# Kernel tuning notes

Measured on AMD Instinct MI355X. Metric: run time of the kernel, lower is better.

## Reference

```python
import jax, jax.numpy as jnp
import numpy as np

B, V, H, R, RULE_DIM, DK, GMLP_H, OUT = 4096, 8, 512, 16, 64, 32, 16, 512
TEMP = float(np.sqrt(DK))  # SelectAttention temperature = sqrt(d_k)
EPS = 1e-10


def gumbel_hard(logits, u, tau=1.0):
    # straight-through hard gumbel-softmax over last axis (F.gumbel_softmax hard=True)
    g = -jnp.log(-jnp.log(u + EPS) + EPS)
    y = jax.nn.softmax((logits + g) / tau, axis=-1)
    hard = jax.nn.one_hot(jnp.argmax(y, axis=-1), y.shape[-1], dtype=y.dtype)
    return hard + y - jax.lax.stop_gradient(y)


def setup_inputs() -> dict:
    key = jax.random.key(0)
    ks = jax.random.split(key, 16)
    s = lambda d: 1.0 / np.sqrt(d)
    return {
        "hidden": jax.random.normal(ks[0], (B, V, H), jnp.float32),
        "u_var": jax.random.uniform(ks[1], (B, V * V), jnp.float32),
        "u_rule": jax.random.uniform(ks[2], (B, R), jnp.float32),
        # variable_rule_select: shared query/key Linear(H, 32)
        "Wq": jax.random.normal(ks[3], (H, DK), jnp.float32) * s(H),
        "bq": jnp.zeros((DK,), jnp.float32),
        "Wk": jax.random.normal(ks[4], (H, DK), jnp.float32) * s(H),
        "bk": jnp.zeros((DK,), jnp.float32),
        # rule embeddings [R, rule_dim]
        "rule_emb": jax.random.normal(ks[5], (R, RULE_DIM), jnp.float32),
        # rule_select_: shared Linear(3H, 32) query, Linear(rule_dim, 32) key
        "Wq2": jax.random.normal(ks[6], (3 * H, DK), jnp.float32) * s(3 * H),
        "bq2": jnp.zeros((DK,), jnp.float32),
        "Wk2": jax.random.normal(ks[7], (RULE_DIM, DK), jnp.float32) * s(RULE_DIM),
        "bk2": jnp.zeros((DK,), jnp.float32),
        # rule_mlp = GroupMLP(2H -> 16 -> input_dim, num=R), GroupLinearLayer has no bias
        "W1": jax.random.normal(ks[8], (R, 2 * H, GMLP_H), jnp.float32) * s(2 * H),
        "W2": jax.random.normal(ks[9], (R, GMLP_H, OUT), jnp.float32) * s(GMLP_H),
    }


def reference(hidden, u_var, u_rule, Wq, bq, Wk, bk, rule_emb, Wq2, bq2, Wk2, bk2, W1, W2):
    b, v, h = hidden.shape
    # variable_rule_select(hidden, hidden): shared Linear projections, bmm scores
    q = hidden @ Wq + bq                                  # [B,V,dk]
    k = hidden @ Wk + bk                                  # [B,V,dk]
    scores = jnp.einsum('bid,bjd->bij', q, k) / TEMP      # [B,V,V]
    # hard gumbel-softmax over flattened V*V pair grid
    mask = gumbel_hard(scores.reshape(b, -1), u_var).reshape(b, v, v)
    mask = mask.transpose(0, 2, 1)                        # mask.permute(0,2,1)
    primary = mask.sum(axis=2)                            # [B,V] one-hot primary variable
    context = mask.sum(axis=1)                            # [B,V] one-hot context variable
    h_p = jnp.einsum('bv,bvh->bh', primary, hidden)       # gather primary slot
    h_c = jnp.einsum('bv,bvh->bh', context, hidden)       # gather context slot
    h_mean = hidden.mean(axis=1)
    # rule_select_: query from concat(primary, context, pooled state) [B,3H]
    q2 = jnp.concatenate([h_p, h_c, h_mean], axis=-1) @ Wq2 + bq2   # [B,dk]
    k2 = rule_emb @ Wk2 + bk2                                        # [R,dk]
    rscores = (q2 @ k2.T) / TEMP                                     # [B,R]
    rmask = gumbel_hard(rscores, u_rule)                             # [B,R] one-hot rule
    # rule_mlp: GroupMLP(2H->16->input_dim) over all rules, then hard dispatch
    comb = jnp.concatenate([h_p, h_c], axis=-1)                      # [B,2H]
    h1 = jax.nn.relu(jnp.einsum('bd,rde->bre', comb, W1))            # [B,R,16]
    rout = jnp.einsum('bre,reo->bro', h1, W2)                        # [B,R,out]
    rule_out = jnp.einsum('br,bro->bo', rmask, rout)                 # [B,out]
    # scatter result back to the selected primary variable slot
    out = primary[:, :, None] * rule_out[:, None, :]                 # [B,V,out]
    return out
```

## Files before the change

kernel.cpp:

```cpp
#include <hip/hip_runtime.h>

#define TEMP 5.656854249492380195f
#define EPSG 1e-10f

#define XSTR 68
#define WSTR 64

__launch_bounds__(256, 2)
__global__ void k1_kernel(const float* __restrict__ hidden,
                          const float* __restrict__ u_var,
                          const float* __restrict__ u_rule,
                          const float* __restrict__ Wq,
                          const float* __restrict__ bq,
                          const float* __restrict__ Wk,
                          const float* __restrict__ bk,
                          const float* __restrict__ rule_emb,
                          const float* __restrict__ Wk2,
                          const float* __restrict__ bk2,
                          const float* __restrict__ Wq2,
                          const float* __restrict__ bq2,
                          int* __restrict__ selbuf,
                          int* __restrict__ rselbuf) {
    const int tid = threadIdx.x;
    const int b0  = blockIdx.x * 8;

    __shared__ float4 smem4[(64 * XSTR + 64 * WSTR) / 4];
    float* smem = reinterpret_cast<float*>(smem4);
    float* xt = smem;
    float* wt = smem + 64 * XSTR;
    __shared__ float  hm[8 * 512];
    __shared__ float  sk2[512];
    __shared__ float4 part4[4][8][8];
    __shared__ float  s_q2[8][32];
    __shared__ int    ssel[8];

    for (int t = tid; t < 512; t += 256) {
        int r = t >> 5, d = t & 31;
        float acc = bk2[d];
        for (int h = 0; h < 64; ++h)
            acc += rule_emb[r * 64 + h] * Wk2[h * 32 + d];
        sk2[t] = acc;
    }

    const int tn = tid & 15;
    const int tm = tid >> 4;

    float4 acc0 = make_float4(0.f, 0.f, 0.f, 0.f);
    float4 acc1 = make_float4(0.f, 0.f, 0.f, 0.f);
    float4 acc2 = make_float4(0.f, 0.f, 0.f, 0.f);
    float4 acc3 = make_float4(0.f, 0.f, 0.f, 0.f);

    for (int c = 0; c < 8; ++c) {
        #pragma unroll
        for (int p = 0; p < 4; ++p) {
            int f   = p * 256 + tid;
            int row = f >> 4;
            int c4  = f & 15;
            int bb  = row >> 3, v = row & 7;
            float4 val = *reinterpret_cast<const float4*>(
                hidden + (size_t)(b0 + bb) * 4096 + v * 512 + c * 64 + c4 * 4);
            *reinterpret_cast<float4*>(&xt[row * XSTR + c4 * 4]) = val;
        }
        #pragma unroll
        for (int p = 0; p < 4; ++p) {
            int f  = p * 256 + tid;
            int k  = f >> 4;
            int n4 = f & 15;
            int h  = c * 64 + k;
            const float* src = (n4 < 8) ? (Wq + h * 32 + n4 * 4)
                                        : (Wk + h * 32 + (n4 - 8) * 4);
            *reinterpret_cast<float4*>(&wt[k * WSTR + n4 * 4]) =
                *reinterpret_cast<const float4*>(src);
        }
        __syncthreads();

        #pragma unroll 4
        for (int k4 = 0; k4 < 16; ++k4) {
            float4 x0 = *reinterpret_cast<const float4*>(&xt[(tm * 4 + 0) * XSTR + k4 * 4]);
            float4 x1 = *reinterpret_cast<const float4*>(&xt[(tm * 4 + 1) * XSTR + k4 * 4]);
            float4 x2 = *reinterpret_cast<const float4*>(&xt[(tm * 4 + 2) * XSTR + k4 * 4]);
            float4 x3 = *reinterpret_cast<const float4*>(&xt[(tm * 4 + 3) * XSTR + k4 * 4]);
            float4 w0 = *reinterpret_cast<const float4*>(&wt[(k4 * 4 + 0) * WSTR + tn * 4]);
            float4 w1 = *reinterpret_cast<const float4*>(&wt[(k4 * 4 + 1) * WSTR + tn * 4]);
            float4 w2 = *reinterpret_cast<const float4*>(&wt[(k4 * 4 + 2) * WSTR + tn * 4]);
            float4 w3 = *reinterpret_cast<const float4*>(&wt[(k4 * 4 + 3) * WSTR + tn * 4]);
            acc0.x += x0.x * w0.x + x0.y * w1.x + x0.z * w2.x + x0.w * w3.x;
            acc0.y += x0.x * w0.y + x0.y * w1.y + x0.z * w2.y + x0.w * w3.y;
            acc0.z += x0.x * w0.z + x0.y * w1.z + x0.z * w2.z + x0.w * w3.z;
            acc0.w += x0.x * w0.w + x0.y * w1.w + x0.z * w2.w + x0.w * w3.w;
            acc1.x += x1.x * w0.x + x1.y * w1.x + x1.z * w2.x + x1.w * w3.x;
            acc1.y += x1.x * w0.y + x1.y * w1.y + x1.z * w2.y + x1.w * w3.y;
            acc1.z += x1.x * w0.z + x1.y * w1.z + x1.z * w2.z + x1.w * w3.z;
            acc1.w += x1.x * w0.w + x1.y * w1.w + x1.z * w2.w + x1.w * w3.w;
            acc2.x += x2.x * w0.x + x2.y * w1.x + x2.z * w2.x + x2.w * w3.x;
            acc2.y += x2.x * w0.y + x2.y * w1.y + x2.z * w2.y + x2.w * w3.y;
            acc2.z += x2.x * w0.z + x2.y * w1.z + x2.z * w2.z + x2.w * w3.z;
            acc2.w += x2.x * w0.w + x2.y * w1.w + x2.z * w2.w + x2.w * w3.w;
            acc3.x += x3.x * w0.x + x3.y * w1.x + x3.z * w2.x + x3.w * w3.x;
            acc3.y += x3.x * w0.y + x3.y * w1.y + x3.z * w2.y + x3.w * w3.y;
            acc3.z += x3.x * w0.z + x3.y * w1.z + x3.z * w2.z + x3.w * w3.z;
            acc3.w += x3.x * w0.w + x3.y * w1.w + x3.z * w2.w + x3.w * w3.w;
        }

        {
            int bb = tid >> 5, hg = tid & 31;
            float m0 = 0.f, m1 = 0.f;
            #pragma unroll
            for (int v = 0; v < 8; ++v) {
                float2 x2 = *reinterpret_cast<const float2*>(&xt[(bb * 8 + v) * XSTR + hg * 2]);
                m0 += x2.x; m1 += x2.y;
            }
            hm[bb * 512 + c * 64 + hg * 2]     = m0 * 0.125f;
            hm[bb * 512 + c * 64 + hg * 2 + 1] = m1 * 0.125f;
        }
        __syncthreads();
    }

    {
        const float* bsrc = (tn < 8) ? (bq + tn * 4) : (bk + (tn - 8) * 4);
        float4 bias4 = *reinterpret_cast<const float4*>(bsrc);
        float4 r0, r1, r2, r3;
        r0.x = acc0.x + bias4.x; r0.y = acc0.y + bias4.y; r0.z = acc0.z + bias4.z; r0.w = acc0.w + bias4.w;
        r1.x = acc1.x + bias4.x; r1.y = acc1.y + bias4.y; r1.z = acc1.z + bias4.z; r1.w = acc1.w + bias4.w;
        r2.x = acc2.x + bias4.x; r2.y = acc2.y + bias4.y; r2.z = acc2.z + bias4.z; r2.w = acc2.w + bias4.w;
        r3.x = acc3.x + bias4.x; r3.y = acc3.y + bias4.y; r3.z = acc3.z + bias4.z; r3.w = acc3.w + bias4.w;
        float* sq = smem;
        *reinterpret_cast<float4*>(&sq[(tm * 4 + 0) * XSTR + tn * 4]) = r0;
        *reinterpret_cast<float4*>(&sq[(tm * 4 + 1) * XSTR + tn * 4]) = r1;
        *reinterpret_cast<float4*>(&sq[(tm * 4 + 2) * XSTR + tn * 4]) = r2;
        *reinterpret_cast<float4*>(&sq[(tm * 4 + 3) * XSTR + tn * 4]) = r3;
    }
    __syncthreads();

    {
        const float* sq = smem;
        const int w    = tid >> 6;
        const int lane = tid & 63;
        #pragma unroll
        for (int half = 0; half < 2; ++half) {
            const int bb = w + half * 4;
            const int b  = b0 + bb;
            const int i = lane >> 3, j = lane & 7;
            float s = 0.f;
            #pragma unroll
            for (int d4 = 0; d4 < 8; ++d4) {
                float4 qv = *reinterpret_cast<const float4*>(&sq[(bb * 8 + i) * XSTR + d4 * 4]);
                float4 kv = *reinterpret_cast<const float4*>(&sq[(bb * 8 + j) * XSTR + 32 + d4 * 4]);
                s += qv.x * kv.x + qv.y * kv.y + qv.z * kv.z + qv.w * kv.w;
            }
            s /= TEMP;
            float u = u_var[(size_t)b * 64 + lane];
            float g = -logf(-logf(u + EPSG) + EPSG);
            float pm = s + g;
            int idx = lane;
            #pragma unroll
            for (int off = 32; off >= 1; off >>= 1) {
                float pv = __shfl_xor(pm, off);
                int   pi = __shfl_xor(idx, off);
                if (pv > pm || (pv == pm && pi < idx)) { pm = pv; idx = pi; }
            }
            if (lane == 0) { selbuf[b] = idx; ssel[bb] = idx; }
        }
    }
    __syncthreads();

    {
        float* comb = smem;
        const float4* h4 = reinterpret_cast<const float4*>(hidden);
        #pragma unroll
        for (int p = 0; p < 8; ++p) {
            int f    = p * 256 + tid;
            int bb   = f >> 8, idx = f & 255;
            int half = idx >> 7, cc = idx & 127;
            int sv   = ssel[bb];
            int row  = half ? (sv >> 3) : (sv & 7);
            reinterpret_cast<float4*>(comb)[bb * 256 + idx] =
                h4[((size_t)(b0 + bb) * 8 + row) * 128 + cc];
        }
    }
    __syncthreads();

    {
        const float* comb = smem;
        const int d4 = tid & 7, s = tid >> 3;
        float4 acc[8];
        #pragma unroll
        for (int bb = 0; bb < 8; ++bb) acc[bb] = make_float4(0.f, 0.f, 0.f, 0.f);

        for (int kt = 0; kt < 6; ++kt) {
            float4 w[8];
            #pragma unroll
            for (int j = 0; j < 8; ++j)
                w[j] = *reinterpret_cast<const float4*>(
                    Wq2 + (size_t)(kt * 256 + s * 8 + j) * 32 + d4 * 4);
            #pragma unroll
            for (int bb = 0; bb < 8; ++bb) {
                const float* xsrc = (kt < 4) ? &comb[bb * 1024 + kt * 256]
                                             : &hm[bb * 512 + (kt - 4) * 256];
                #pragma unroll
                for (int j = 0; j < 8; ++j) {
                    float x = xsrc[s * 8 + j];
                    acc[bb].x += x * w[j].x;
                    acc[bb].y += x * w[j].y;
                    acc[bb].z += x * w[j].z;
                    acc[bb].w += x * w[j].w;
                }
            }
        }
        #pragma unroll
        for (int off = 8; off < 64; off <<= 1) {
            #pragma unroll
            for (int bb = 0; bb < 8; ++bb) {
                acc[bb].x += __shfl_xor(acc[bb].x, off);
                acc[bb].y += __shfl_xor(acc[bb].y, off);
                acc[bb].z += __shfl_xor(acc[bb].z, off);
                acc[bb].w += __shfl_xor(acc[bb].w, off);
            }
        }
        if ((s & 7) == 0) {
            #pragma unroll
            for (int bb = 0; bb < 8; ++bb) part4[tid >> 6][bb][d4] = acc[bb];
        }
    }
    __syncthreads();
    {
        const int bb = tid >> 5, col = tid & 31;
        float q2 = bq2[col];
        #pragma unroll
        for (int wv = 0; wv < 4; ++wv) {
            const float* pf = reinterpret_cast<const float*>(&part4[wv][bb][col >> 2]);
            q2 += pf[col & 3];
        }
        s_q2[bb][col] = q2;
    }
    __syncthreads();
    if (tid < 128) {
        const int bb = tid >> 4, r = tid & 15;
        const int b = b0 + bb;
        float sc = 0.f;
        #pragma unroll
        for (int d = 0; d < 32; ++d) sc += s_q2[bb][d] * sk2[r * 32 + d];
        sc /= TEMP;
        float u = u_rule[(size_t)b * 16 + r];
        float g = -logf(-logf(u + EPSG) + EPSG);
        float pm = sc + g;
        int idx = r;
        #pragma unroll
        for (int off = 8; off >= 1; off >>= 1) {
            float pv = __shfl_xor(pm, off, 16);
            int   pi = __shfl_xor(idx, off, 16);
            if (pv > pm || (pv == pm && pi < idx)) { pm = pv; idx = pi; }
        }
        if (r == 0) rselbuf[b] = idx;
    }
}

__launch_bounds__(256, 4)
__global__ void k3_kernel(const float* __restrict__ hidden,
                          const float* __restrict__ W1,
                          const float* __restrict__ W2,
                          const int* __restrict__ selbuf,
                          const int* __restrict__ rselbuf,
                          float* __restrict__ outbuf) {
    const int tid = threadIdx.x;
    const int b   = blockIdx.x;

    __shared__ float comb[1024];
    __shared__ float part[4][16];
    __shared__ float s_h1[16];
    __shared__ float s_rout[512];

    const int sv = selbuf[b];
    const int r  = rselbuf[b];
    const int js = sv & 7, cs = sv >> 3;

    {
        const float4* h4 = reinterpret_cast<const float4*>(hidden);
        float4 v;
        if (tid < 128) v = h4[((size_t)b * 8 + js) * 128 + tid];
        else           v = h4[((size_t)b * 8 + cs) * 128 + (tid - 128)];
        *reinterpret_cast<float4*>(&comb[tid * 4]) = v;
    }
    __syncthreads();

    {
        const int e  = tid & 15;
        const int sl = tid >> 4;
        const float* w1p = W1 + (size_t)r * 16384;
        float a = 0.f;
        for (int i = 0; i < 64; ++i) {
            int rr = i * 16 + sl;
            a += comb[rr] * w1p[rr * 16 + e];
        }
        a += __shfl_xor(a, 16);
        a += __shfl_xor(a, 32);
        if ((sl & 3) == 0) part[sl >> 2][e] = a;
    }
    __syncthreads();
    if (tid < 16)
        s_h1[tid] = fmaxf(part[0][tid] + part[1][tid] + part[2][tid] + part[3][tid], 0.f);
    __syncthreads();

    {
        const float* w2 = W2 + (size_t)r * 8192;
        int o0 = tid * 2;
        float a0 = 0.f, a1 = 0.f;
        #pragma unroll
        for (int ee = 0; ee < 16; ++ee) {
            float h1e = s_h1[ee];
            float2 ww = *reinterpret_cast<const float2*>(w2 + ee * 512 + o0);
            a0 += h1e * ww.x;
            a1 += h1e * ww.y;
        }
        s_rout[o0]     = a0;
        s_rout[o0 + 1] = a1;
    }
    __syncthreads();

    {
        const int v    = tid >> 5;
        const int col0 = (tid & 31) * 16;
        float4 z = make_float4(0.f, 0.f, 0.f, 0.f);
        float4 r0 = z, r1 = z, r2 = z, r3 = z;
        if (v == js) {
            r0 = *reinterpret_cast<const float4*>(&s_rout[col0]);
            r1 = *reinterpret_cast<const float4*>(&s_rout[col0 + 4]);
            r2 = *reinterpret_cast<const float4*>(&s_rout[col0 + 8]);
            r3 = *reinterpret_cast<const float4*>(&s_rout[col0 + 12]);
        }
        float* ob = outbuf + (size_t)b * 4096 + v * 512 + col0;
        *reinterpret_cast<float4*>(ob)      = r0;
        *reinterpret_cast<float4*>(ob + 4)  = r1;
        *reinterpret_cast<float4*>(ob + 8)  = r2;
        *reinterpret_cast<float4*>(ob + 12) = r3;
    }
}

extern "C" void kernel_launch(void* const* d_in, const int* in_sizes, int n_in,
                              void* d_out, int out_size, void* d_ws, size_t ws_size,
                              hipStream_t stream) {
    const float* hidden   = (const float*)d_in[0];
    const float* u_var    = (const float*)d_in[1];
    const float* u_rule   = (const float*)d_in[2];
    const float* Wq       = (const float*)d_in[3];
    const float* bq       = (const float*)d_in[4];
    const float* Wk       = (const float*)d_in[5];
    const float* bk       = (const float*)d_in[6];
    const float* rule_emb = (const float*)d_in[7];
    const float* Wq2      = (const float*)d_in[8];
    const float* bq2      = (const float*)d_in[9];
    const float* Wk2      = (const float*)d_in[10];
    const float* bk2      = (const float*)d_in[11];
    const float* W1       = (const float*)d_in[12];
    const float* W2       = (const float*)d_in[13];

    char* ws = (char*)d_ws;
    int*   sel  = (int*)(ws + 4096);
    int*   rsel = (int*)(ws + 20480);
    float* outf = (float*)d_out;

    hipLaunchKernelGGL(k1_kernel, dim3(512), dim3(256), 0, stream,
                       hidden, u_var, u_rule, Wq, bq, Wk, bk,
                       rule_emb, Wk2, bk2, Wq2, bq2, sel, rsel);
    hipLaunchKernelGGL(k3_kernel, dim3(4096), dim3(256), 0, stream,
                       hidden, W1, W2, sel, rsel, outf);
}
```

Before: 90.39 us.

## Double-buffer QK projection staging with direct global-to-LDS loads

Restructures the Q/K projection loop into 16 smaller 32-wide K chunks with two LDS buffers, issuing the next chunk's hidden and weight loads before computing on the current one. Where available it uses the global_load_lds builtin to write directly into shared memory without passing through registers. This aims to hide global-load latency behind the FMA loop, but it drops the padded row strides, which may bring back LDS bank conflicts, and the loop now runs twice as many iterations, each ending in a barrier.

```diff
diff --git a/kernel.cpp b/kernel.cpp
--- a/kernel.cpp
+++ b/kernel.cpp
@@ -3,8 +3,26 @@
 #define TEMP 5.656854249492380195f
 #define EPSG 1e-10f
 
-#define XSTR 68
-#define WSTR 64
+#define KCH 32
+
+#if defined(__has_builtin)
+#if __has_builtin(__builtin_amdgcn_global_load_lds)
+#define HAVE_GLL 1
+#endif
+#endif
+
+__device__ __forceinline__ void stage_f4(const float* gp, float* lp_base, int lane) {
+#ifdef HAVE_GLL
+    (void)lane;
+    __builtin_amdgcn_global_load_lds(
+        (const __attribute__((address_space(1))) unsigned int*)(gp),
+        (__attribute__((address_space(3))) unsigned int*)(lp_base),
+        16, 0, 0);
+#else
+    float4 v = *reinterpret_cast<const float4*>(gp);
+    *reinterpret_cast<float4*>(lp_base + lane * 4) = v;
+#endif
+}
 
 __launch_bounds__(256, 2)
 __global__ void k1_kernel(const float* __restrict__ hidden,
@@ -24,11 +42,8 @@
     const int tid = threadIdx.x;
     const int b0  = blockIdx.x * 8;
 
-    __shared__ float4 smem4[(64 * XSTR + 64 * WSTR) / 4];
-    float* smem = reinterpret_cast<float*>(smem4);
-    float* xt = smem;
-    float* wt = smem + 64 * XSTR;
-    __shared__ float  hm[8 * 512];
+    __shared__ float  smem[8192];
+    __shared__ float  hm[4096];
     __shared__ float  sk2[512];
     __shared__ float4 part4[4][8][8];
     __shared__ float  s_q2[8][32];
@@ -42,48 +57,59 @@
         sk2[t] = acc;
     }
 
-    const int tn = tid & 15;
-    const int tm = tid >> 4;
+    const int w    = tid >> 6;
+    const int lane = tid & 63;
+    const int tn   = tid & 15;
+    const int tm   = tid >> 4;
 
     float4 acc0 = make_float4(0.f, 0.f, 0.f, 0.f);
     float4 acc1 = make_float4(0.f, 0.f, 0.f, 0.f);
     float4 acc2 = make_float4(0.f, 0.f, 0.f, 0.f);
     float4 acc3 = make_float4(0.f, 0.f, 0.f, 0.f);
 
-    for (int c = 0; c < 8; ++c) {
-        #pragma unroll
-        for (int p = 0; p < 4; ++p) {
-            int f   = p * 256 + tid;
-            int row = f >> 4;
-            int c4  = f & 15;
-            int bb  = row >> 3, v = row & 7;
-            float4 val = *reinterpret_cast<const float4*>(
-                hidden + (size_t)(b0 + bb) * 4096 + v * 512 + c * 64 + c4 * 4);
-            *reinterpret_cast<float4*>(&xt[row * XSTR + c4 * 4]) = val;
-        }
-        #pragma unroll
-        for (int p = 0; p < 4; ++p) {
-            int f  = p * 256 + tid;
-            int k  = f >> 4;
-            int n4 = f & 15;
-            int h  = c * 64 + k;
-            const float* src = (n4 < 8) ? (Wq + h * 32 + n4 * 4)
-                                        : (Wk + h * 32 + (n4 - 8) * 4);
-            *reinterpret_cast<float4*>(&wt[k * WSTR + n4 * 4]) =
-                *reinterpret_cast<const float4*>(src);
-        }
-        __syncthreads();
+    #define STAGE_CHUNK(c_, p_)                                               \
+    do {                                                                      \
+        _Pragma("unroll")                                                     \
+        for (int i = 0; i < 2; ++i) {                                         \
+            int f   = w * 128 + i * 64 + lane;            \
+            int row = f >> 3, c4 = f & 7;                                     \
+            const float* gp = hidden + (size_t)(b0 + (row >> 3)) * 4096       \
+                              + (row & 7) * 512 + (c_) * KCH + c4 * 4;        \
+            stage_f4(gp, &smem[(p_) * 4096 + (w * 128 + i * 64) * 4], lane);  \
+        }                                                                     \
+        _Pragma("unroll")                                                     \
+        for (int i = 0; i < 2; ++i) {                                         \
+            int f  = w * 128 + i * 64 + lane;             \
+            int k  = f >> 4, n4 = f & 15;                                     \
+            const float* gp = (n4 < 8)                                        \
+                ? (Wq + (size_t)((c_) * KCH + k) * 32 + n4 * 4)               \
+                : (Wk + (size_t)((c_) * KCH + k) * 32 + (n4 - 8) * 4);        \
+            stage_f4(gp, &smem[(p_) * 4096 + 2048 + (w * 128 + i * 64) * 4],  \
+                     lane);                                                   \
+        }                                                                     \
+    } while (0)
+
+    STAGE_CHUNK(0, 0);
+    __syncthreads();
+
+    for (int c = 0; c < 16; ++c) {
+        const int p = c & 1;
+
+        if (c < 15) STAGE_CHUNK(c + 1, p ^ 1);
+
+        const float* xt = &smem[p * 4096];
+        const float* wt = &smem[p * 4096 + 2048];
 
         #pragma unroll 4
-        for (int k4 = 0; k4 < 16; ++k4) {
-            float4 x0 = *reinterpret_cast<const float4*>(&xt[(tm * 4 + 0) * XSTR + k4 * 4]);
-            float4 x1 = *reinterpret_cast<const float4*>(&xt[(tm * 4 + 1) * XSTR + k4 * 4]);
-            float4 x2 = *reinterpret_cast<const float4*>(&xt[(tm * 4 + 2) * XSTR + k4 * 4]);
-            float4 x3 = *reinterpret_cast<const float4*>(&xt[(tm * 4 + 3) * XSTR + k4 * 4]);
-            float4 w0 = *reinterpret_cast<const float4*>(&wt[(k4 * 4 + 0) * WSTR + tn * 4]);
-            float4 w1 = *reinterpret_cast<const float4*>(&wt[(k4 * 4 + 1) * WSTR + tn * 4]);
-            float4 w2 = *reinterpret_cast<const float4*>(&wt[(k4 * 4 + 2) * WSTR + tn * 4]);
-            float4 w3 = *reinterpret_cast<const float4*>(&wt[(k4 * 4 + 3) * WSTR + tn * 4]);
+        for (int k4 = 0; k4 < 8; ++k4) {
+            float4 x0 = *reinterpret_cast<const float4*>(&xt[(tm * 4 + 0) * 32 + k4 * 4]);
+            float4 x1 = *reinterpret_cast<const float4*>(&xt[(tm * 4 + 1) * 32 + k4 * 4]);
+            float4 x2 = *reinterpret_cast<const float4*>(&xt[(tm * 4 + 2) * 32 + k4 * 4]);
+            float4 x3 = *reinterpret_cast<const float4*>(&xt[(tm * 4 + 3) * 32 + k4 * 4]);
+            float4 w0 = *reinterpret_cast<const float4*>(&wt[(k4 * 4 + 0) * 64 + tn * 4]);
+            float4 w1 = *reinterpret_cast<const float4*>(&wt[(k4 * 4 + 1) * 64 + tn * 4]);
+            float4 w2 = *reinterpret_cast<const float4*>(&wt[(k4 * 4 + 2) * 64 + tn * 4]);
+            float4 w3 = *reinterpret_cast<const float4*>(&wt[(k4 * 4 + 3) * 64 + tn * 4]);
             acc0.x += x0.x * w0.x + x0.y * w1.x + x0.z * w2.x + x0.w * w3.x;
             acc0.y += x0.x * w0.y + x0.y * w1.y + x0.z * w2.y + x0.w * w3.y;
             acc0.z += x0.x * w0.z + x0.y * w1.z + x0.z * w2.z + x0.w * w3.z;
@@ -104,14 +130,10 @@
 
         {
             int bb = tid >> 5, hg = tid & 31;
-            float m0 = 0.f, m1 = 0.f;
-            #pragma unroll
-            for (int v = 0; v < 8; ++v) {
-                float2 x2 = *reinterpret_cast<const float2*>(&xt[(bb * 8 + v) * XSTR + hg * 2]);
-                m0 += x2.x; m1 += x2.y;
-            }
-            hm[bb * 512 + c * 64 + hg * 2]     = m0 * 0.125f;
-            hm[bb * 512 + c * 64 + hg * 2 + 1] = m1 * 0.125f;
+            float m = 0.f;
+            #pragma unroll
+            for (int v = 0; v < 8; ++v) m += xt[(bb * 8 + v) * 32 + hg];
+            hm[bb * 512 + c * KCH + hg] = m * 0.125f;
         }
         __syncthreads();
     }
@@ -125,17 +147,15 @@
         r2.x = acc2.x + bias4.x; r2.y = acc2.y + bias4.y; r2.z = acc2.z + bias4.z; r2.w = acc2.w + bias4.w;
         r3.x = acc3.x + bias4.x; r3.y = acc3.y + bias4.y; r3.z = acc3.z + bias4.z; r3.w = acc3.w + bias4.w;
         float* sq = smem;
-        *reinterpret_cast<float4*>(&sq[(tm * 4 + 0) * XSTR + tn * 4]) = r0;
-        *reinterpret_cast<float4*>(&sq[(tm * 4 + 1) * XSTR + tn * 4]) = r1;
-        *reinterpret_cast<float4*>(&sq[(tm * 4 + 2) * XSTR + tn * 4]) = r2;
-        *reinterpret_cast<float4*>(&sq[(tm * 4 + 3) * XSTR + tn * 4]) = r3;
+        *reinterpret_cast<float4*>(&sq[(tm * 4 + 0) * 64 + tn * 4]) = r0;
+        *reinterpret_cast<float4*>(&sq[(tm * 4 + 1) * 64 + tn * 4]) = r1;
+        *reinterpret_cast<float4*>(&sq[(tm * 4 + 2) * 64 + tn * 4]) = r2;
+        *reinterpret_cast<float4*>(&sq[(tm * 4 + 3) * 64 + tn * 4]) = r3;
     }
     __syncthreads();
 
     {
         const float* sq = smem;
-        const int w    = tid >> 6;
-        const int lane = tid & 63;
         #pragma unroll
         for (int half = 0; half < 2; ++half) {
             const int bb = w + half * 4;
@@ -144,8 +164,8 @@
             float s = 0.f;
             #pragma unroll
             for (int d4 = 0; d4 < 8; ++d4) {
-                float4 qv = *reinterpret_cast<const float4*>(&sq[(bb * 8 + i) * XSTR + d4 * 4]);
-                float4 kv = *reinterpret_cast<const float4*>(&sq[(bb * 8 + j) * XSTR + 32 + d4 * 4]);
+                float4 qv = *reinterpret_cast<const float4*>(&sq[(bb * 8 + i) * 64 + d4 * 4]);
+                float4 kv = *reinterpret_cast<const float4*>(&sq[(bb * 8 + j) * 64 + 32 + d4 * 4]);
                 s += qv.x * kv.x + qv.y * kv.y + qv.z * kv.z + qv.w * kv.w;
             }
             s /= TEMP;
@@ -188,10 +208,10 @@
         for (int bb = 0; bb < 8; ++bb) acc[bb] = make_float4(0.f, 0.f, 0.f, 0.f);
 
         for (int kt = 0; kt < 6; ++kt) {
-            float4 w[8];
+            float4 wv[8];
             #pragma unroll
             for (int j = 0; j < 8; ++j)
-                w[j] = *reinterpret_cast<const float4*>(
+                wv[j] = *reinterpret_cast<const float4*>(
                     Wq2 + (size_t)(kt * 256 + s * 8 + j) * 32 + d4 * 4);
             #pragma unroll
             for (int bb = 0; bb < 8; ++bb) {
@@ -200,10 +220,10 @@
                 #pragma unroll
                 for (int j = 0; j < 8; ++j) {
                     float x = xsrc[s * 8 + j];
-                    acc[bb].x += x * w[j].x;
-                    acc[bb].y += x * w[j].y;
-                    acc[bb].z += x * w[j].z;
-                    acc[bb].w += x * w[j].w;
+                    acc[bb].x += x * wv[j].x;
+                    acc[bb].y += x * wv[j].y;
+                    acc[bb].z += x * wv[j].z;
+                    acc[bb].w += x * wv[j].w;
                 }
             }
         }
@@ -227,8 +247,8 @@
         const int bb = tid >> 5, col = tid & 31;
         float q2 = bq2[col];
         #pragma unroll
-        for (int wv = 0; wv < 4; ++wv) {
-            const float* pf = reinterpret_cast<const float*>(&part4[wv][bb][col >> 2]);
+        for (int wv2 = 0; wv2 < 4; ++wv2) {
+            const float* pf = reinterpret_cast<const float*>(&part4[wv2][bb][col >> 2]);
             q2 += pf[col & 3];
         }
         s_q2[bb][col] = q2;
```

New measurement: 97.02 us. 7.3% more time.

## Fuse rule-MLP and output scatter into the selection kernel

Applied to the files above, without the earlier changes.

Merges the second kernel (group MLP on the selected rule plus the scatter into the output) into the first kernel. Each wavefront now handles two batch rows, reusing the gathered primary/context vectors already held in shared memory and keeping the selections in shared memory instead of a workspace buffer. This removes a kernel launch, the workspace round trip and the second read of hidden. In exchange, the MLP and the output writes run on only 512 blocks instead of 4096, which lowers parallelism for the W1 gather and the output store phase.

```diff
diff --git a/kernel.cpp b/kernel.cpp
--- a/kernel.cpp
+++ b/kernel.cpp
@@ -7,20 +7,21 @@
 #define WSTR 64
 
 __launch_bounds__(256, 2)
-__global__ void k1_kernel(const float* __restrict__ hidden,
-                          const float* __restrict__ u_var,
-                          const float* __restrict__ u_rule,
-                          const float* __restrict__ Wq,
-                          const float* __restrict__ bq,
-                          const float* __restrict__ Wk,
-                          const float* __restrict__ bk,
-                          const float* __restrict__ rule_emb,
-                          const float* __restrict__ Wk2,
-                          const float* __restrict__ bk2,
-                          const float* __restrict__ Wq2,
-                          const float* __restrict__ bq2,
-                          int* __restrict__ selbuf,
-                          int* __restrict__ rselbuf) {
+__global__ void fused_kernel(const float* __restrict__ hidden,
+                             const float* __restrict__ u_var,
+                             const float* __restrict__ u_rule,
+                             const float* __restrict__ Wq,
+                             const float* __restrict__ bq,
+                             const float* __restrict__ Wk,
+                             const float* __restrict__ bk,
+                             const float* __restrict__ rule_emb,
+                             const float* __restrict__ Wk2,
+                             const float* __restrict__ bk2,
+                             const float* __restrict__ Wq2,
+                             const float* __restrict__ bq2,
+                             const float* __restrict__ W1,
+                             const float* __restrict__ W2,
+                             float* __restrict__ outbuf) {
     const int tid = threadIdx.x;
     const int b0  = blockIdx.x * 8;
 
@@ -33,6 +34,7 @@
     __shared__ float4 part4[4][8][8];
     __shared__ float  s_q2[8][32];
     __shared__ int    ssel[8];
+    __shared__ int    s_rsel[8];
 
     for (int t = tid; t < 512; t += 256) {
         int r = t >> 5, d = t & 31;
@@ -42,8 +44,10 @@
         sk2[t] = acc;
     }
 
-    const int tn = tid & 15;
-    const int tm = tid >> 4;
+    const int w    = tid >> 6;
+    const int lane = tid & 63;
+    const int tn   = tid & 15;
+    const int tm   = tid >> 4;
 
     float4 acc0 = make_float4(0.f, 0.f, 0.f, 0.f);
     float4 acc1 = make_float4(0.f, 0.f, 0.f, 0.f);
@@ -134,8 +138,6 @@
 
     {
         const float* sq = smem;
-        const int w    = tid >> 6;
-        const int lane = tid & 63;
         #pragma unroll
         for (int half = 0; half < 2; ++half) {
             const int bb = w + half * 4;
@@ -159,7 +161,7 @@
                 int   pi = __shfl_xor(idx, off);
                 if (pv > pm || (pv == pm && pi < idx)) { pm = pv; idx = pi; }
             }
-            if (lane == 0) { selbuf[b] = idx; ssel[bb] = idx; }
+            if (lane == 0) ssel[bb] = idx;
         }
     }
     __syncthreads();
@@ -188,10 +190,10 @@
         for (int bb = 0; bb < 8; ++bb) acc[bb] = make_float4(0.f, 0.f, 0.f, 0.f);
 
         for (int kt = 0; kt < 6; ++kt) {
-            float4 w[8];
+            float4 wv[8];
             #pragma unroll
             for (int j = 0; j < 8; ++j)
-                w[j] = *reinterpret_cast<const float4*>(
+                wv[j] = *reinterpret_cast<const float4*>(
                     Wq2 + (size_t)(kt * 256 + s * 8 + j) * 32 + d4 * 4);
             #pragma unroll
             for (int bb = 0; bb < 8; ++bb) {
@@ -200,10 +202,10 @@
                 #pragma unroll
                 for (int j = 0; j < 8; ++j) {
                     float x = xsrc[s * 8 + j];
-                    acc[bb].x += x * w[j].x;
-                    acc[bb].y += x * w[j].y;
-                    acc[bb].z += x * w[j].z;
-                    acc[bb].w += x * w[j].w;
+                    acc[bb].x += x * wv[j].x;
+                    acc[bb].y += x * wv[j].y;
+                    acc[bb].z += x * wv[j].z;
+                    acc[bb].w += x * wv[j].w;
                 }
             }
         }
@@ -227,8 +229,8 @@
         const int bb = tid >> 5, col = tid & 31;
         float q2 = bq2[col];
         #pragma unroll
-        for (int wv = 0; wv < 4; ++wv) {
-            const float* pf = reinterpret_cast<const float*>(&part4[wv][bb][col >> 2]);
+        for (int wv2 = 0; wv2 < 4; ++wv2) {
+            const float* pf = reinterpret_cast<const float*>(&part4[wv2][bb][col >> 2]);
             q2 += pf[col & 3];
         }
         s_q2[bb][col] = q2;
@@ -251,88 +253,59 @@
             int   pi = __shfl_xor(idx, off, 16);
             if (pv > pm || (pv == pm && pi < idx)) { pm = pv; idx = pi; }
         }
-        if (r == 0) rselbuf[b] = idx;
-    }
-}
-
-__launch_bounds__(256, 4)
-__global__ void k3_kernel(const float* __restrict__ hidden,
-                          const float* __restrict__ W1,
-                          const float* __restrict__ W2,
-                          const int* __restrict__ selbuf,
-                          const int* __restrict__ rselbuf,
-                          float* __restrict__ outbuf) {
-    const int tid = threadIdx.x;
-    const int b   = blockIdx.x;
-
-    __shared__ float comb[1024];
-    __shared__ float part[4][16];
-    __shared__ float s_h1[16];
-    __shared__ float s_rout[512];
-
-    const int sv = selbuf[b];
-    const int r  = rselbuf[b];
-    const int js = sv & 7, cs = sv >> 3;
-
-    {
-        const float4* h4 = reinterpret_cast<const float4*>(hidden);
-        float4 v;
-        if (tid < 128) v = h4[((size_t)b * 8 + js) * 128 + tid];
-        else           v = h4[((size_t)b * 8 + cs) * 128 + (tid - 128)];
-        *reinterpret_cast<float4*>(&comb[tid * 4]) = v;
-    }
-    __syncthreads();
-
-    {
-        const int e  = tid & 15;
-        const int sl = tid >> 4;
-        const float* w1p = W1 + (size_t)r * 16384;
-        float a = 0.f;
-        for (int i = 0; i < 64; ++i) {
-            int rr = i * 16 + sl;
-            a += comb[rr] * w1p[rr * 16 + e];
-        }
-        a += __shfl_xor(a, 16);
-        a += __shfl_xor(a, 32);
-        if ((sl & 3) == 0) part[sl >> 2][e] = a;
-    }
-    __syncthreads();
-    if (tid < 16)
-        s_h1[tid] = fmaxf(part[0][tid] + part[1][tid] + part[2][tid] + part[3][tid], 0.f);
-    __syncthreads();
-
-    {
-        const float* w2 = W2 + (size_t)r * 8192;
-        int o0 = tid * 2;
-        float a0 = 0.f, a1 = 0.f;
-        #pragma unroll
-        for (int ee = 0; ee < 16; ++ee) {
-            float h1e = s_h1[ee];
-            float2 ww = *reinterpret_cast<const float2*>(w2 + ee * 512 + o0);
-            a0 += h1e * ww.x;
-            a1 += h1e * ww.y;
-        }
-        s_rout[o0]     = a0;
-        s_rout[o0 + 1] = a1;
-    }
-    __syncthreads();
-
-    {
-        const int v    = tid >> 5;
-        const int col0 = (tid & 31) * 16;
-        float4 z = make_float4(0.f, 0.f, 0.f, 0.f);
-        float4 r0 = z, r1 = z, r2 = z, r3 = z;
-        if (v == js) {
-            r0 = *reinterpret_cast<const float4*>(&s_rout[col0]);
-            r1 = *reinterpret_cast<const float4*>(&s_rout[col0 + 4]);
-            r2 = *reinterpret_cast<const float4*>(&s_rout[col0 + 8]);
-            r3 = *reinterpret_cast<const float4*>(&s_rout[col0 + 12]);
-        }
-        float* ob = outbuf + (size_t)b * 4096 + v * 512 + col0;
-        *reinterpret_cast<float4*>(ob)      = r0;
-        *reinterpret_cast<float4*>(ob + 4)  = r1;
-        *reinterpret_cast<float4*>(ob + 8)  = r2;
-        *reinterpret_cast<float4*>(ob + 12) = r3;
+        if (r == 0) s_rsel[bb] = idx;
+    }
+    __syncthreads();
+
+    {
+        const float* comb = smem;
+        #pragma unroll
+        for (int half = 0; half < 2; ++half) {
+            const int bb = w + half * 4;
+            const int b  = b0 + bb;
+            const int sv = ssel[bb];
+            const int js = sv & 7;
+            const int r  = s_rsel[bb];
+
+            const int e  = lane & 15;
+            const int sl = lane >> 4;
+            const float* cb  = comb + bb * 1024;
+            const float* w1p = W1 + (size_t)r * 16384 + e;
+
+            float a0 = 0.f, a1 = 0.f, a2 = 0.f, a3 = 0.f;
+            for (int i = 0; i < 64; ++i) {
+                int rr = i * 16 + sl * 4;
+                a0 += cb[rr + 0] * w1p[(size_t)(rr + 0) * 16];
+                a1 += cb[rr + 1] * w1p[(size_t)(rr + 1) * 16];
+                a2 += cb[rr + 2] * w1p[(size_t)(rr + 2) * 16];
+                a3 += cb[rr + 3] * w1p[(size_t)(rr + 3) * 16];
+            }
+            float a = (a0 + a1) + (a2 + a3);
+            a += __shfl_xor(a, 16);
+            a += __shfl_xor(a, 32);
+            a = fmaxf(a, 0.f);
+
+            const float* w2 = W2 + (size_t)r * 8192 + lane * 8;
+            float4 oA = make_float4(0.f, 0.f, 0.f, 0.f);
+            float4 oB = make_float4(0.f, 0.f, 0.f, 0.f);
+            #pragma unroll
+            for (int ee = 0; ee < 16; ++ee) {
+                float he = __shfl(a, ee);
+                float4 wa = *reinterpret_cast<const float4*>(w2 + ee * 512);
+                float4 wb = *reinterpret_cast<const float4*>(w2 + ee * 512 + 4);
+                oA.x += he * wa.x; oA.y += he * wa.y; oA.z += he * wa.z; oA.w += he * wa.w;
+                oB.x += he * wb.x; oB.y += he * wb.y; oB.z += he * wb.z; oB.w += he * wb.w;
+            }
+
+            float4 z = make_float4(0.f, 0.f, 0.f, 0.f);
+            float* ob = outbuf + (size_t)b * 4096 + lane * 8;
+            #pragma unroll
+            for (int v = 0; v < 8; ++v) {
+                bool hit = (v == js);
+                *reinterpret_cast<float4*>(ob + v * 512)     = hit ? oA : z;
+                *reinterpret_cast<float4*>(ob + v * 512 + 4) = hit ? oB : z;
+            }
+        }
     }
 }
 
@@ -354,14 +327,9 @@
     const float* W1       = (const float*)d_in[12];
     const float* W2       = (const float*)d_in[13];
 
-    char* ws = (char*)d_ws;
-    int*   sel  = (int*)(ws + 4096);
-    int*   rsel = (int*)(ws + 20480);
     float* outf = (float*)d_out;
 
-    hipLaunchKernelGGL(k1_kernel, dim3(512), dim3(256), 0, stream,
+    hipLaunchKernelGGL(fused_kernel, dim3(512), dim3(256), 0, stream,
                        hidden, u_var, u_rule, Wq, bq, Wk, bk,
-                       rule_emb, Wk2, bk2, Wq2, bq2, sel, rsel);
-    hipLaunchKernelGGL(k3_kernel, dim3(4096), dim3(256), 0, stream,
-                       hidden, W1, W2, sel, rsel, outf);
+                       rule_emb, Wk2, bk2, Wq2, bq2, W1, W2, outf);
 }
```

Result: no change. 90.15 us (-0.3%).
